# Optimization experiments

Measured on AMD Instinct MI355X. Metric: run time of the kernel, lower is better.

Reference implementation:

```python
import jax, jax.numpy as jnp
import numpy as np

HIDDEN = 1024   # hidden_dimensions (dim_in)
NUM_HEADS = 16
HEAD_DIM = 64   # dim_q == dim_k == output_dimensions per head
BATCH = 4
SEQ = 2048


def setup_inputs() -> dict:
    key = jax.random.key(0)
    ks = jax.random.split(key, 11)
    s = 1.0 / np.sqrt(HIDDEN)
    so = 1.0 / np.sqrt(NUM_HEADS * HEAD_DIM)
    return {
        "Q": jax.random.normal(ks[0], (BATCH, SEQ, HIDDEN), jnp.float32),
        "K": jax.random.normal(ks[1], (BATCH, SEQ, HIDDEN), jnp.float32),
        "V": jax.random.normal(ks[2], (BATCH, SEQ, HIDDEN), jnp.float32),
        # per-head projection weights stacked over the head axis
        "Wq": jax.random.uniform(ks[3], (NUM_HEADS, HIDDEN, HEAD_DIM), jnp.float32, -s, s),
        "bq": jax.random.uniform(ks[4], (NUM_HEADS, HEAD_DIM), jnp.float32, -s, s),
        "Wk": jax.random.uniform(ks[5], (NUM_HEADS, HIDDEN, HEAD_DIM), jnp.float32, -s, s),
        "bk": jax.random.uniform(ks[6], (NUM_HEADS, HEAD_DIM), jnp.float32, -s, s),
        "Wv": jax.random.uniform(ks[7], (NUM_HEADS, HIDDEN, HEAD_DIM), jnp.float32, -s, s),
        "bv": jax.random.uniform(ks[8], (NUM_HEADS, HEAD_DIM), jnp.float32, -s, s),
        # output projection: concat(num_heads*head_dim) -> hidden
        "Wo": jax.random.uniform(ks[9], (NUM_HEADS * HEAD_DIM, HIDDEN), jnp.float32, -so, so),
        "bo": jax.random.uniform(ks[10], (HIDDEN,), jnp.float32, -so, so),
    }


def reference(Q, K, V, Wq, bq, Wk, bk, Wv, bv, Wo, bo):
    # Per-head linear projections (batched over heads instead of Python loop)
    q = jnp.einsum("bsd,hdk->bhsk", Q, Wq) + bq[None, :, None, :]  # [B,H,S,dk]
    k = jnp.einsum("bsd,hdk->bhsk", K, Wk) + bk[None, :, None, :]
    v = jnp.einsum("bsd,hdk->bhsk", V, Wv) + bv[None, :, None, :]
    # Scaled dot-product attention
    scale = 1.0 / jnp.sqrt(jnp.asarray(k.shape[-1], q.dtype))
    scores = jnp.einsum("bhqk,bhsk->bhqs", q, k) * scale          # [B,H,S,S]
    attn = jax.nn.softmax(scores, axis=-1)
    o = jnp.einsum("bhqs,bhsk->bhqk", attn, v)                     # [B,H,S,dk]
    # Concatenate heads along the feature dim, then output linear
    B, H, S, dk = o.shape
    concat = jnp.transpose(o, (0, 2, 1, 3)).reshape(B, S, H * dk)  # [B,S,H*dk]
    return concat @ Wo + bo                                        # [B,S,HIDDEN]
```

## Files before the change

kernel.cpp:

```cpp
#include <hip/hip_runtime.h>
#include <hip/hip_bf16.h>
#include <stdint.h>

typedef unsigned short u16;
typedef uint32_t u32;
typedef __attribute__((ext_vector_type(4))) float f32x4;
typedef __attribute__((ext_vector_type(16))) float f32x16;
typedef __attribute__((ext_vector_type(8))) short s8v;
typedef __attribute__((ext_vector_type(4))) unsigned short u16x4;
typedef __attribute__((ext_vector_type(2))) uint32_t u32x2;

#define SCALE_Q 0.18033688f

__device__ __forceinline__ u16 f2bf(float f) {
  union { float f; uint32_t u; } v; v.f = f;
  uint32_t r = v.u + 0x7fffu + ((v.u >> 16) & 1u);
  return (u16)(r >> 16);
}

__device__ __forceinline__ u32 pk2(float lo, float hi) {
  __hip_bfloat162 h = __float22bfloat162_rn(float2{lo, hi});
  union { __hip_bfloat162 h; u32 u; } c; c.h = h; return c.u;
}

__device__ __forceinline__ void gl16(const void* g, void* l) {
  __builtin_amdgcn_global_load_lds((const __attribute__((address_space(1))) u32*)g,
                                   (__attribute__((address_space(3))) u32*)l, 16, 0, 0);
}

#define BARRIER()  __builtin_amdgcn_s_barrier()
#define SCHEDB()   __builtin_amdgcn_sched_barrier(0)

__global__ __launch_bounds__(256) void k_conv3(const float* __restrict__ a, const float* __restrict__ b,
                                               const float* __restrict__ c, u16* __restrict__ oa,
                                               u16* __restrict__ ob, u16* __restrict__ oc) {
  int which = blockIdx.y;
  const float* in = which == 0 ? a : (which == 1 ? b : c);
  u16* out = which == 0 ? oa : (which == 1 ? ob : oc);
  int i = (blockIdx.x * 256 + threadIdx.x) * 4;
  float4 v = *(const float4*)(in + i);
  u16x4 o; o[0] = f2bf(v.x); o[1] = f2bf(v.y); o[2] = f2bf(v.z); o[3] = f2bf(v.w);
  *(u16x4*)(out + i) = o;
}

__global__ __launch_bounds__(256) void k_convW_t(const float* __restrict__ wq, const float* __restrict__ wk,
                                                 const float* __restrict__ wv, u16* __restrict__ oq,
                                                 u16* __restrict__ ok, u16* __restrict__ ov) {
  __shared__ float T[64][65];
  const int z = blockIdx.z, h = blockIdx.y, d0 = blockIdx.x * 64;
  const float* w = z == 0 ? wq : (z == 1 ? wk : wv);
  u16* o = z == 0 ? oq : (z == 1 ? ok : ov);
  const float scale = z == 0 ? SCALE_Q : 1.0f;
  const int t = threadIdx.x;
#pragma unroll
  for (int i = 0; i < 16; ++i) {
    int f = t + i * 256;
    T[f >> 6][f & 63] = w[(h * 1024 + d0 + (f >> 6)) * 64 + (f & 63)];
  }
  __syncthreads();
#pragma unroll
  for (int i = 0; i < 16; ++i) {
    int g = t + i * 256;
    o[(h * 64 + (g >> 6)) * 1024 + d0 + (g & 63)] = f2bf(T[g & 63][g >> 6] * scale);
  }
}

__global__ __launch_bounds__(256) void k_convWo_t(const float* __restrict__ w, u16* __restrict__ o) {
  __shared__ float T[64][65];
  const int n0 = blockIdx.x * 64, c0 = blockIdx.y * 64;
  const int t = threadIdx.x;
#pragma unroll
  for (int i = 0; i < 16; ++i) {
    int f = t + i * 256;
    T[f >> 6][f & 63] = w[(c0 + (f >> 6)) * 1024 + n0 + (f & 63)];
  }
  __syncthreads();
#pragma unroll
  for (int i = 0; i < 16; ++i) {
    int g = t + i * 256;
    o[(n0 + (g >> 6)) * 1024 + c0 + (g & 63)] = f2bf(T[g & 63][g >> 6]);
  }
}

__global__ __launch_bounds__(256) void k_gemm3(
    const u16* __restrict__ Aq, const u16* __restrict__ Ak, const u16* __restrict__ Av,
    const u16* __restrict__ Bq, const u16* __restrict__ Bk, const u16* __restrict__ Bv,
    const float* __restrict__ bqp, const float* __restrict__ bkp, const float* __restrict__ bvp,
    u16* __restrict__ oq, u16* __restrict__ ok, u16* __restrict__ ov) {
  constexpr int Kd = 1024, Nd = 1024;
  __shared__ alignas(16) u16 As[2][128 * 64];
  __shared__ alignas(16) u16 Bs[2][128 * 64];
  const int z = blockIdx.z;
  const u16* A = z == 0 ? Aq : (z == 1 ? Ak : Av);
  const u16* Bt = z == 0 ? Bq : (z == 1 ? Bk : Bv);
  const float* bias = z == 0 ? bqp : (z == 1 ? bkp : bvp);

  const int t = threadIdx.x;
  const int lane = t & 63;
  const int w = t >> 6;
  const int wm = w >> 1, wn = w & 1;
  const int lr = lane & 15, lg = lane >> 4;
  const long bm = blockIdx.x * 128, bn = blockIdx.y * 128;
  const int r8 = lane >> 3, c8 = lane & 7;
  const int chunk = c8 ^ r8;

  f32x4 acc[4][4] = {};
  const u16* Ap = A + (bm + w * 8 + r8) * (long)Kd + chunk * 8;
  const u16* Bp = Bt + (bn + w * 8 + r8) * (long)Kd + chunk * 8;

  auto GSTAGE = [&](u16* Asb, u16* Bsb, int kt) {
#pragma unroll
    for (int p = 0; p < 4; ++p) {
      gl16(Ap + (long)p * 32 * Kd + kt, Asb + (p * 32 + w * 8) * 64);
      gl16(Bp + (long)p * 32 * Kd + kt, Bsb + (p * 32 + w * 8) * 64);
    }
  };
  auto GCOMP = [&](const u16* Asb, const u16* Bsb) {
#pragma unroll
    for (int ks = 0; ks < 2; ++ks) {
      s8v af[4], bf[4];
#pragma unroll
      for (int i = 0; i < 4; ++i) {
        int arow = wm * 64 + i * 16 + lr;
        af[i] = *(const s8v*)(Asb + arow * 64 + (((ks * 4 + lg) ^ (arow & 7)) * 8));
        int brow = wn * 64 + i * 16 + lr;
        bf[i] = *(const s8v*)(Bsb + brow * 64 + (((ks * 4 + lg) ^ (brow & 7)) * 8));
      }
#pragma unroll
      for (int i = 0; i < 4; ++i)
#pragma unroll
        for (int j = 0; j < 4; ++j)
          acc[i][j] = __builtin_amdgcn_mfma_f32_16x16x32_bf16(af[i], bf[j], acc[i][j], 0, 0, 0);
    }
  };

  GSTAGE(As[0], Bs[0], 0);
  for (int kt = 0; kt < 16; ++kt) {
    BARRIER();
    SCHEDB();
    if (kt < 15) {
      GSTAGE(As[(kt + 1) & 1], Bs[(kt + 1) & 1], (kt + 1) * 64);
      asm volatile("s_waitcnt vmcnt(8)" ::: "memory");
    } else {
      asm volatile("s_waitcnt vmcnt(0)" ::: "memory");
    }
    SCHEDB();
    BARRIER();
    SCHEDB();
    GCOMP(As[kt & 1], Bs[kt & 1]);
  }

  const float bscale = z == 0 ? SCALE_Q : 1.0f;
  float bcol[4];
#pragma unroll
  for (int j = 0; j < 4; ++j) bcol[j] = bias[bn + wn * 64 + j * 16 + lr] * bscale;

  if (z < 2) {
    u16* C = z == 0 ? oq : ok;
#pragma unroll
    for (int i = 0; i < 4; ++i) {
      long m0 = bm + wm * 64 + i * 16 + lg * 4;
#pragma unroll
      for (int j = 0; j < 4; ++j) {
        long n = bn + wn * 64 + j * 16 + lr;
#pragma unroll
        for (int r = 0; r < 4; ++r)
          C[(m0 + r) * Nd + n] = f2bf(acc[i][j][r] + bcol[j]);
      }
    }
  } else {
    u16* C = ov;
    int lgp = ((lg & 1) << 1) | (lg >> 1);
#pragma unroll
    for (int i = 0; i < 4; ++i) {
      long m0 = bm + wm * 64 + i * 16 + lgp * 4;
      int b = (int)(m0 >> 11), s0 = (int)(m0 & 2047);
#pragma unroll
      for (int j = 0; j < 4; ++j) {
        int n = (int)(bn + wn * 64 + j * 16 + lr);
        int h = n >> 6, dv = n & 63;
        u32x2 cc;
        cc[0] = pk2(acc[i][j][0] + bcol[j], acc[i][j][1] + bcol[j]);
        cc[1] = pk2(acc[i][j][2] + bcol[j], acc[i][j][3] + bcol[j]);
        *(u32x2*)(C + (long)((b * 16 + h) * 64 + dv) * 2048 + s0) = cc;
      }
    }
  }
}

__global__ __launch_bounds__(256) void k_gemmo(const u16* __restrict__ A, const u16* __restrict__ Bt,
                                               const float* __restrict__ bias, float* __restrict__ C) {
  constexpr int Kd = 1024, Nd = 1024;
  __shared__ alignas(16) u16 As[2][128 * 64];
  __shared__ alignas(16) u16 Bs[2][128 * 64];
  const int t = threadIdx.x;
  const int lane = t & 63;
  const int w = t >> 6;
  const int wm = w >> 1, wn = w & 1;
  const int lr = lane & 15, lg = lane >> 4;
  const long bm = blockIdx.x * 128, bn = blockIdx.y * 128;
  const int r8 = lane >> 3, c8 = lane & 7;
  const int chunk = c8 ^ r8;

  f32x4 acc[4][4] = {};
  const u16* Ap = A + (bm + w * 8 + r8) * (long)Kd + chunk * 8;
  const u16* Bp = Bt + (bn + w * 8 + r8) * (long)Kd + chunk * 8;

  auto GSTAGE = [&](u16* Asb, u16* Bsb, int kt) {
#pragma unroll
    for (int p = 0; p < 4; ++p) {
      gl16(Ap + (long)p * 32 * Kd + kt, Asb + (p * 32 + w * 8) * 64);
      gl16(Bp + (long)p * 32 * Kd + kt, Bsb + (p * 32 + w * 8) * 64);
    }
  };
  auto GCOMP = [&](const u16* Asb, const u16* Bsb) {
#pragma unroll
    for (int ks = 0; ks < 2; ++ks) {
      s8v af[4], bf[4];
#pragma unroll
      for (int i = 0; i < 4; ++i) {
        int arow = wm * 64 + i * 16 + lr;
        af[i] = *(const s8v*)(Asb + arow * 64 + (((ks * 4 + lg) ^ (arow & 7)) * 8));
        int brow = wn * 64 + i * 16 + lr;
        bf[i] = *(const s8v*)(Bsb + brow * 64 + (((ks * 4 + lg) ^ (brow & 7)) * 8));
      }
#pragma unroll
      for (int i = 0; i < 4; ++i)
#pragma unroll
        for (int j = 0; j < 4; ++j)
          acc[i][j] = __builtin_amdgcn_mfma_f32_16x16x32_bf16(af[i], bf[j], acc[i][j], 0, 0, 0);
    }
  };

  GSTAGE(As[0], Bs[0], 0);
  for (int kt = 0; kt < 16; ++kt) {
    BARRIER();
    SCHEDB();
    if (kt < 15) {
      GSTAGE(As[(kt + 1) & 1], Bs[(kt + 1) & 1], (kt + 1) * 64);
      asm volatile("s_waitcnt vmcnt(8)" ::: "memory");
    } else {
      asm volatile("s_waitcnt vmcnt(0)" ::: "memory");
    }
    SCHEDB();
    BARRIER();
    SCHEDB();
    GCOMP(As[kt & 1], Bs[kt & 1]);
  }

  float bcol[4];
#pragma unroll
  for (int j = 0; j < 4; ++j) bcol[j] = bias[bn + wn * 64 + j * 16 + lr];
#pragma unroll
  for (int i = 0; i < 4; ++i) {
    long m0 = bm + wm * 64 + i * 16 + lg * 4;
#pragma unroll
    for (int j = 0; j < 4; ++j) {
      long n = bn + wn * 64 + j * 16 + lr;
#pragma unroll
      for (int r = 0; r < 4; ++r)
        C[(m0 + r) * Nd + n] = acc[i][j][r] + bcol[j];
    }
  }
}

__global__ __launch_bounds__(256, 2) void k_attn(const u16* __restrict__ q, const u16* __restrict__ k,
                                                 const u16* __restrict__ vT, u16* __restrict__ o) {
  __shared__ alignas(16) u16 Ks[4][64 * 64];
  __shared__ alignas(16) u16 Vs[4][64 * 64];
  const int t = threadIdx.x;
  const int lane = t & 63;
  const int wv = t >> 6;
  const int l5 = lane & 31, hi = lane >> 5;
  const int r8 = lane >> 3, c8 = lane & 7;
  const int rx = l5 & 7;

  const int wg = blockIdx.x;
  const int ob = (wg & 7) * 64 + (wg >> 3);
  const int qt = ob & 7, h = (ob >> 3) & 15, b = ob >> 7;

  const int qrow0 = qt * 256 + wv * 64 + l5;
  const u16* qpA = q + ((long)(b * 2048 + qrow0) * 1024 + h * 64);
  const u16* qpB = qpA + 32 * 1024;
  s8v qfA[4], qfB[4];
#pragma unroll
  for (int s = 0; s < 4; ++s) {
    qfA[s] = *(const s8v*)(qpA + s * 16 + hi * 8);
    qfB[s] = *(const s8v*)(qpB + s * 16 + hi * 8);
  }

  const u16* Kpp = k + (long)b * 2048 * 1024 + h * 64 + (long)r8 * 1024 + ((c8 ^ r8) * 8);
  const u16* Vpp = vT + (long)(b * 16 + h) * 131072 + (long)r8 * 2048 + ((c8 ^ r8) * 8);

  f32x16 accA0 = {}, accA1 = {}, accB0 = {}, accB1 = {};
  float lA = 0.f, lB = 0.f;

  int offs[4];
#pragma unroll
  for (int s = 0; s < 4; ++s) offs[s] = ((2 * s + hi) ^ rx) * 8;
  const int rb0 = l5 * 64, rb1 = rb0 + 2048;

  auto ASTAGE = [&](int buf, int kv) {
#pragma unroll
    for (int r0 = 0; r0 < 2; ++r0) {
      int rowo = wv * 16 + r0 * 8;
      gl16(Kpp + ((long)kv + rowo) * 1024, &Ks[buf][rowo * 64]);
      gl16(Vpp + (long)rowo * 2048 + kv,   &Vs[buf][rowo * 64]);
    }
  };

  auto ATILE = [&](int buf) {
    const u16* Ksb = Ks[buf];
    const u16* Vsb = Vs[buf];
    s8v kf0[4], kf1[4];
#pragma unroll
    for (int s = 0; s < 4; ++s) {
      kf0[s] = *(const s8v*)(Ksb + rb0 + offs[s]);
      kf1[s] = *(const s8v*)(Ksb + rb1 + offs[s]);
    }
    f32x16 sA0 = {}, sA1 = {}, sB0 = {}, sB1 = {};
    __builtin_amdgcn_s_setprio(1);
#pragma unroll
    for (int s = 0; s < 4; ++s) {
      sA0 = __builtin_amdgcn_mfma_f32_32x32x16_bf16(kf0[s], qfA[s], sA0, 0, 0, 0);
      sA1 = __builtin_amdgcn_mfma_f32_32x32x16_bf16(kf1[s], qfA[s], sA1, 0, 0, 0);
      sB0 = __builtin_amdgcn_mfma_f32_32x32x16_bf16(kf0[s], qfB[s], sB0, 0, 0, 0);
      sB1 = __builtin_amdgcn_mfma_f32_32x32x16_bf16(kf1[s], qfB[s], sB1, 0, 0, 0);
    }
    __builtin_amdgcn_s_setprio(0);
    u32 PA[16], PB[16];
#pragma unroll
    for (int kb = 0; kb < 2; ++kb) {
#pragma unroll
      for (int r1 = 0; r1 < 4; ++r1) {
        float a0 = __builtin_amdgcn_exp2f(kb ? sA1[4 * r1 + 0] : sA0[4 * r1 + 0]);
        float a1 = __builtin_amdgcn_exp2f(kb ? sA1[4 * r1 + 1] : sA0[4 * r1 + 1]);
        float a2 = __builtin_amdgcn_exp2f(kb ? sA1[4 * r1 + 2] : sA0[4 * r1 + 2]);
        float a3 = __builtin_amdgcn_exp2f(kb ? sA1[4 * r1 + 3] : sA0[4 * r1 + 3]);
        lA += (a0 + a1) + (a2 + a3);
        PA[kb * 8 + r1 * 2 + 0] = pk2(a0, a1);
        PA[kb * 8 + r1 * 2 + 1] = pk2(a2, a3);
        float b0 = __builtin_amdgcn_exp2f(kb ? sB1[4 * r1 + 0] : sB0[4 * r1 + 0]);
        float b1 = __builtin_amdgcn_exp2f(kb ? sB1[4 * r1 + 1] : sB0[4 * r1 + 1]);
        float b2 = __builtin_amdgcn_exp2f(kb ? sB1[4 * r1 + 2] : sB0[4 * r1 + 2]);
        float b3 = __builtin_amdgcn_exp2f(kb ? sB1[4 * r1 + 3] : sB0[4 * r1 + 3]);
        lB += (b0 + b1) + (b2 + b3);
        PB[kb * 8 + r1 * 2 + 0] = pk2(b0, b1);
        PB[kb * 8 + r1 * 2 + 1] = pk2(b2, b3);
      }
    }
    __builtin_amdgcn_s_setprio(1);
#pragma unroll
    for (int s2 = 0; s2 < 4; ++s2) {
      union { s8v v; u32 w[4]; } pa, pb;
      pa.w[0] = PA[4 * s2 + 0]; pa.w[1] = PA[4 * s2 + 1];
      pa.w[2] = PA[4 * s2 + 2]; pa.w[3] = PA[4 * s2 + 3];
      pb.w[0] = PB[4 * s2 + 0]; pb.w[1] = PB[4 * s2 + 1];
      pb.w[2] = PB[4 * s2 + 2]; pb.w[3] = PB[4 * s2 + 3];
      s8v vf0 = *(const s8v*)(Vsb + rb0 + offs[s2]);
      s8v vf1 = *(const s8v*)(Vsb + rb1 + offs[s2]);
      accA0 = __builtin_amdgcn_mfma_f32_32x32x16_bf16(vf0, pa.v, accA0, 0, 0, 0);
      accA1 = __builtin_amdgcn_mfma_f32_32x32x16_bf16(vf1, pa.v, accA1, 0, 0, 0);
      accB0 = __builtin_amdgcn_mfma_f32_32x32x16_bf16(vf0, pb.v, accB0, 0, 0, 0);
      accB1 = __builtin_amdgcn_mfma_f32_32x32x16_bf16(vf1, pb.v, accB1, 0, 0, 0);
    }
    __builtin_amdgcn_s_setprio(0);
  };

  ASTAGE(0, 0);
  ASTAGE(1, 64);
  asm volatile("s_waitcnt vmcnt(4)" ::: "memory");
  SCHEDB();
  BARRIER();
  SCHEDB();
  for (int tt = 0; tt < 30; ++tt) {
    ASTAGE((tt + 2) & 3, (tt + 2) * 64);
    ATILE(tt & 3);
    asm volatile("s_waitcnt vmcnt(4) lgkmcnt(0)" ::: "memory");
    SCHEDB();
    BARRIER();
    SCHEDB();
  }
  ATILE(30 & 3);
  asm volatile("s_waitcnt vmcnt(0) lgkmcnt(0)" ::: "memory");
  SCHEDB();
  BARRIER();
  SCHEDB();
  ATILE(31 & 3);

  lA += __shfl_xor(lA, 32);
  lB += __shfl_xor(lB, 32);
  float iA = 1.0f / lA, iB = 1.0f / lB;
  u16* opA = o + ((long)(b * 2048 + qrow0) * 1024 + h * 64);
  u16* opB = opA + 32 * 1024;
#pragma unroll
  for (int kb = 0; kb < 2; ++kb) {
#pragma unroll
    for (int r1 = 0; r1 < 4; ++r1) {
      u32x2 ca, cb;
      float a0 = kb ? accA1[4 * r1 + 0] : accA0[4 * r1 + 0];
      float a1 = kb ? accA1[4 * r1 + 1] : accA0[4 * r1 + 1];
      float a2 = kb ? accA1[4 * r1 + 2] : accA0[4 * r1 + 2];
      float a3 = kb ? accA1[4 * r1 + 3] : accA0[4 * r1 + 3];
      ca[0] = pk2(a0 * iA, a1 * iA);
      ca[1] = pk2(a2 * iA, a3 * iA);
      *(u32x2*)(opA + kb * 32 + r1 * 8 + hi * 4) = ca;
      float b0 = kb ? accB1[4 * r1 + 0] : accB0[4 * r1 + 0];
      float b1 = kb ? accB1[4 * r1 + 1] : accB0[4 * r1 + 1];
      float b2 = kb ? accB1[4 * r1 + 2] : accB0[4 * r1 + 2];
      float b3 = kb ? accB1[4 * r1 + 3] : accB0[4 * r1 + 3];
      cb[0] = pk2(b0 * iB, b1 * iB);
      cb[1] = pk2(b2 * iB, b3 * iB);
      *(u32x2*)(opB + kb * 32 + r1 * 8 + hi * 4) = cb;
    }
  }
}

extern "C" void kernel_launch(void* const* d_in, const int* in_sizes, int n_in,
                              void* d_out, int out_size, void* d_ws, size_t ws_size,
                              hipStream_t stream) {
  const float* Q  = (const float*)d_in[0];
  const float* K  = (const float*)d_in[1];
  const float* V  = (const float*)d_in[2];
  const float* Wq = (const float*)d_in[3];
  const float* bq = (const float*)d_in[4];
  const float* Wk = (const float*)d_in[5];
  const float* bk = (const float*)d_in[6];
  const float* Wv = (const float*)d_in[7];
  const float* bvp = (const float*)d_in[8];
  const float* Wo = (const float*)d_in[9];
  const float* bo = (const float*)d_in[10];
  float* out = (float*)d_out;

  char* ws = (char*)d_ws;
  const size_t MB16 = (size_t)8192 * 1024 * 2;
  u16* Qb  = (u16*)(ws);
  u16* Kb  = (u16*)(ws + MB16);
  u16* Vb  = (u16*)(ws + 2 * MB16);
  u16* WqT = (u16*)(ws + 3 * MB16);
  u16* WkT = (u16*)(ws + 3 * MB16 + ((size_t)2 << 20));
  u16* WvT = (u16*)(ws + 3 * MB16 + ((size_t)4 << 20));
  u16* WoT = (u16*)(ws + 3 * MB16 + ((size_t)6 << 20));
  u16* qws = (u16*)(ws + 3 * MB16 + ((size_t)8 << 20));
  u16* kws = (u16*)(ws + 4 * MB16 + ((size_t)8 << 20));
  u16* vTs = (u16*)(ws + 5 * MB16 + ((size_t)8 << 20));
  u16* ows = Qb;

  k_conv3<<<dim3(8192, 3), 256, 0, stream>>>(Q, K, V, Qb, Kb, Vb);
  k_convW_t<<<dim3(16, 16, 3), 256, 0, stream>>>(Wq, Wk, Wv, WqT, WkT, WvT);
  k_convWo_t<<<dim3(16, 16), 256, 0, stream>>>(Wo, WoT);

  k_gemm3<<<dim3(64, 8, 3), 256, 0, stream>>>(Qb, Kb, Vb, WqT, WkT, WvT,
                                              bq, bk, bvp, qws, kws, vTs);

  k_attn<<<dim3(512), 256, 0, stream>>>(qws, kws, vTs, ows);

  k_gemmo<<<dim3(64, 8), 256, 0, stream>>>(ows, WoT, bo, out);
}
```

Baseline: 204.7 us.

## Interleave softmax exp with MFMA groups inside attention tile via sched_group_barrier

Splits each attention tile into halves so the exp2/pack work of one half of the score block overlaps the MFMAs of the other half (the second QK^T half and the first PV half). sched_group_barrier masks pin the mix of MFMA, VALU and LDS-read instructions. V fragments are loaded up front and the setprio calls are dropped. The aim is to hide the exp VALU latency behind matrix-core work, at the cost of higher register pressure and a fragile dependence on compiler scheduling.

```diff
diff --git a/kernel.cpp b/kernel.cpp
--- a/kernel.cpp
+++ b/kernel.cpp
@@ -12,6 +12,8 @@
 
 #define SCALE_Q 0.18033688f
 
+union PU { s8v v; u32 w[4]; };
+
 __device__ __forceinline__ u16 f2bf(float f) {
   union { float f; uint32_t u; } v; v.f = f;
   uint32_t r = v.u + 0x7fffu + ((v.u >> 16) & 1u);
@@ -30,6 +32,7 @@
 
 #define BARRIER()  __builtin_amdgcn_s_barrier()
 #define SCHEDB()   __builtin_amdgcn_sched_barrier(0)
+#define SGB(m, n)  __builtin_amdgcn_sched_group_barrier((m), (n), 0)
 
 __global__ __launch_bounds__(256) void k_conv3(const float* __restrict__ a, const float* __restrict__ b,
                                                const float* __restrict__ c, u16* __restrict__ oa,
@@ -309,62 +312,78 @@
     }
   };
 
+  auto EXPPACK = [&](const f32x16& sv, PU& u0, PU& u1, float& l) {
+#pragma unroll
+    for (int r1 = 0; r1 < 4; ++r1) {
+      float p0 = __builtin_amdgcn_exp2f(sv[4 * r1 + 0]);
+      float p1 = __builtin_amdgcn_exp2f(sv[4 * r1 + 1]);
+      float p2 = __builtin_amdgcn_exp2f(sv[4 * r1 + 2]);
+      float p3 = __builtin_amdgcn_exp2f(sv[4 * r1 + 3]);
+      l += (p0 + p1) + (p2 + p3);
+      if (r1 < 2) {
+        u0.w[(r1 & 1) * 2 + 0] = pk2(p0, p1);
+        u0.w[(r1 & 1) * 2 + 1] = pk2(p2, p3);
+      } else {
+        u1.w[(r1 & 1) * 2 + 0] = pk2(p0, p1);
+        u1.w[(r1 & 1) * 2 + 1] = pk2(p2, p3);
+      }
+    }
+  };
+
   auto ATILE = [&](int buf) {
     const u16* Ksb = Ks[buf];
     const u16* Vsb = Vs[buf];
+    PU paU[4], pbU[4];
+    f32x16 sA0 = {}, sB0 = {}, sA1 = {}, sB1 = {};
     s8v kf0[4], kf1[4];
 #pragma unroll
     for (int s = 0; s < 4; ++s) {
       kf0[s] = *(const s8v*)(Ksb + rb0 + offs[s]);
       kf1[s] = *(const s8v*)(Ksb + rb1 + offs[s]);
     }
-    f32x16 sA0 = {}, sA1 = {}, sB0 = {}, sB1 = {};
-    __builtin_amdgcn_s_setprio(1);
 #pragma unroll
     for (int s = 0; s < 4; ++s) {
       sA0 = __builtin_amdgcn_mfma_f32_32x32x16_bf16(kf0[s], qfA[s], sA0, 0, 0, 0);
+      sB0 = __builtin_amdgcn_mfma_f32_32x32x16_bf16(kf0[s], qfB[s], sB0, 0, 0, 0);
+    }
+#pragma unroll
+    for (int g = 0; g < 4; ++g) { SGB(0x100, 2); SGB(0x8, 2); }
+    SCHEDB();
+#pragma unroll
+    for (int s = 0; s < 4; ++s) {
       sA1 = __builtin_amdgcn_mfma_f32_32x32x16_bf16(kf1[s], qfA[s], sA1, 0, 0, 0);
-      sB0 = __builtin_amdgcn_mfma_f32_32x32x16_bf16(kf0[s], qfB[s], sB0, 0, 0, 0);
       sB1 = __builtin_amdgcn_mfma_f32_32x32x16_bf16(kf1[s], qfB[s], sB1, 0, 0, 0);
     }
-    __builtin_amdgcn_s_setprio(0);
-    u32 PA[16], PB[16];
-#pragma unroll
-    for (int kb = 0; kb < 2; ++kb) {
-#pragma unroll
-      for (int r1 = 0; r1 < 4; ++r1) {
-        float a0 = __builtin_amdgcn_exp2f(kb ? sA1[4 * r1 + 0] : sA0[4 * r1 + 0]);
-        float a1 = __builtin_amdgcn_exp2f(kb ? sA1[4 * r1 + 1] : sA0[4 * r1 + 1]);
-        float a2 = __builtin_amdgcn_exp2f(kb ? sA1[4 * r1 + 2] : sA0[4 * r1 + 2]);
-        float a3 = __builtin_amdgcn_exp2f(kb ? sA1[4 * r1 + 3] : sA0[4 * r1 + 3]);
-        lA += (a0 + a1) + (a2 + a3);
-        PA[kb * 8 + r1 * 2 + 0] = pk2(a0, a1);
-        PA[kb * 8 + r1 * 2 + 1] = pk2(a2, a3);
-        float b0 = __builtin_amdgcn_exp2f(kb ? sB1[4 * r1 + 0] : sB0[4 * r1 + 0]);
-        float b1 = __builtin_amdgcn_exp2f(kb ? sB1[4 * r1 + 1] : sB0[4 * r1 + 1]);
-        float b2 = __builtin_amdgcn_exp2f(kb ? sB1[4 * r1 + 2] : sB0[4 * r1 + 2]);
-        float b3 = __builtin_amdgcn_exp2f(kb ? sB1[4 * r1 + 3] : sB0[4 * r1 + 3]);
-        lB += (b0 + b1) + (b2 + b3);
-        PB[kb * 8 + r1 * 2 + 0] = pk2(b0, b1);
-        PB[kb * 8 + r1 * 2 + 1] = pk2(b2, b3);
-      }
-    }
-    __builtin_amdgcn_s_setprio(1);
-#pragma unroll
-    for (int s2 = 0; s2 < 4; ++s2) {
-      union { s8v v; u32 w[4]; } pa, pb;
-      pa.w[0] = PA[4 * s2 + 0]; pa.w[1] = PA[4 * s2 + 1];
-      pa.w[2] = PA[4 * s2 + 2]; pa.w[3] = PA[4 * s2 + 3];
-      pb.w[0] = PB[4 * s2 + 0]; pb.w[1] = PB[4 * s2 + 1];
-      pb.w[2] = PB[4 * s2 + 2]; pb.w[3] = PB[4 * s2 + 3];
-      s8v vf0 = *(const s8v*)(Vsb + rb0 + offs[s2]);
-      s8v vf1 = *(const s8v*)(Vsb + rb1 + offs[s2]);
-      accA0 = __builtin_amdgcn_mfma_f32_32x32x16_bf16(vf0, pa.v, accA0, 0, 0, 0);
-      accA1 = __builtin_amdgcn_mfma_f32_32x32x16_bf16(vf1, pa.v, accA1, 0, 0, 0);
-      accB0 = __builtin_amdgcn_mfma_f32_32x32x16_bf16(vf0, pb.v, accB0, 0, 0, 0);
-      accB1 = __builtin_amdgcn_mfma_f32_32x32x16_bf16(vf1, pb.v, accB1, 0, 0, 0);
-    }
-    __builtin_amdgcn_s_setprio(0);
+    EXPPACK(sA0, paU[0], paU[1], lA);
+    EXPPACK(sB0, pbU[0], pbU[1], lB);
+#pragma unroll
+    for (int g = 0; g < 8; ++g) { SGB(0x8, 1); SGB(0x2, 9); }
+    SCHEDB();
+    s8v vf0[4], vf1[4];
+#pragma unroll
+    for (int s = 0; s < 4; ++s) {
+      vf0[s] = *(const s8v*)(Vsb + rb0 + offs[s]);
+      vf1[s] = *(const s8v*)(Vsb + rb1 + offs[s]);
+    }
+#pragma unroll
+    for (int s2 = 0; s2 < 2; ++s2) {
+      accA0 = __builtin_amdgcn_mfma_f32_32x32x16_bf16(vf0[s2], paU[s2].v, accA0, 0, 0, 0);
+      accA1 = __builtin_amdgcn_mfma_f32_32x32x16_bf16(vf1[s2], paU[s2].v, accA1, 0, 0, 0);
+      accB0 = __builtin_amdgcn_mfma_f32_32x32x16_bf16(vf0[s2], pbU[s2].v, accB0, 0, 0, 0);
+      accB1 = __builtin_amdgcn_mfma_f32_32x32x16_bf16(vf1[s2], pbU[s2].v, accB1, 0, 0, 0);
+    }
+    EXPPACK(sA1, paU[2], paU[3], lA);
+    EXPPACK(sB1, pbU[2], pbU[3], lB);
+#pragma unroll
+    for (int g = 0; g < 8; ++g) { SGB(0x100, 1); SGB(0x8, 1); SGB(0x2, 9); }
+    SCHEDB();
+#pragma unroll
+    for (int s2 = 2; s2 < 4; ++s2) {
+      accA0 = __builtin_amdgcn_mfma_f32_32x32x16_bf16(vf0[s2], paU[s2].v, accA0, 0, 0, 0);
+      accA1 = __builtin_amdgcn_mfma_f32_32x32x16_bf16(vf1[s2], paU[s2].v, accA1, 0, 0, 0);
+      accB0 = __builtin_amdgcn_mfma_f32_32x32x16_bf16(vf0[s2], pbU[s2].v, accB0, 0, 0, 0);
+      accB1 = __builtin_amdgcn_mfma_f32_32x32x16_bf16(vf1[s2], pbU[s2].v, accB1, 0, 0, 0);
+    }
   };
 
   ASTAGE(0, 0);
```

New measurement: 200.8 us. About the same (-1.9%).

## Load K/V fragments directly from global into registers, dropping LDS staging

Applied to the files above, without the earlier changes.

The attention kernel stops staging K and V tiles in LDS through async global-to-LDS copies and barriers. Each wave now loads its own K and V MFMA fragments straight from global memory into registers, double-buffered over 32-key chunks. This removes LDS traffic and block-wide barriers. The cost is that all four waves of a block redundantly fetch the same K/V data from global/L2, with less coalesced 16-byte row-strided accesses and more register pressure.

```diff
diff --git a/kernel.cpp b/kernel.cpp
--- a/kernel.cpp
+++ b/kernel.cpp
@@ -11,6 +11,8 @@
 typedef __attribute__((ext_vector_type(2))) uint32_t u32x2;
 
 #define SCALE_Q 0.18033688f
+
+union PU { s8v v; u32 w[4]; };
 
 __device__ __forceinline__ u16 f2bf(float f) {
   union { float f; uint32_t u; } v; v.f = f;
@@ -266,14 +268,10 @@
 
 __global__ __launch_bounds__(256, 2) void k_attn(const u16* __restrict__ q, const u16* __restrict__ k,
                                                  const u16* __restrict__ vT, u16* __restrict__ o) {
-  __shared__ alignas(16) u16 Ks[4][64 * 64];
-  __shared__ alignas(16) u16 Vs[4][64 * 64];
   const int t = threadIdx.x;
   const int lane = t & 63;
   const int wv = t >> 6;
   const int l5 = lane & 31, hi = lane >> 5;
-  const int r8 = lane >> 3, c8 = lane & 7;
-  const int rx = l5 & 7;
 
   const int wg = blockIdx.x;
   const int ob = (wg & 7) * 64 + (wg >> 3);
@@ -289,104 +287,67 @@
     qfB[s] = *(const s8v*)(qpB + s * 16 + hi * 8);
   }
 
-  const u16* Kpp = k + (long)b * 2048 * 1024 + h * 64 + (long)r8 * 1024 + ((c8 ^ r8) * 8);
-  const u16* Vpp = vT + (long)(b * 16 + h) * 131072 + (long)r8 * 2048 + ((c8 ^ r8) * 8);
+  const u16* Kl = k + (long)b * 2048 * 1024 + h * 64 + (long)l5 * 1024 + hi * 8;
+  const u16* Vl = vT + (long)(b * 16 + h) * 131072 + (long)l5 * 2048 + hi * 8;
 
   f32x16 accA0 = {}, accA1 = {}, accB0 = {}, accB1 = {};
   float lA = 0.f, lB = 0.f;
 
-  int offs[4];
-#pragma unroll
-  for (int s = 0; s < 4; ++s) offs[s] = ((2 * s + hi) ^ rx) * 8;
-  const int rb0 = l5 * 64, rb1 = rb0 + 2048;
-
-  auto ASTAGE = [&](int buf, int kv) {
-#pragma unroll
-    for (int r0 = 0; r0 < 2; ++r0) {
-      int rowo = wv * 16 + r0 * 8;
-      gl16(Kpp + ((long)kv + rowo) * 1024, &Ks[buf][rowo * 64]);
-      gl16(Vpp + (long)rowo * 2048 + kv,   &Vs[buf][rowo * 64]);
-    }
-  };
-
-  auto ATILE = [&](int buf) {
-    const u16* Ksb = Ks[buf];
-    const u16* Vsb = Vs[buf];
-    s8v kf0[4], kf1[4];
+  struct KV { s8v kf[4]; s8v vf[2][2]; };
+  KV b0, b1;
+
+  auto LOAD = [&](KV& bb, int kv0) {
+#pragma unroll
+    for (int s = 0; s < 4; ++s)
+      bb.kf[s] = *(const s8v*)(Kl + (long)kv0 * 1024 + s * 16);
+#pragma unroll
+    for (int d = 0; d < 2; ++d)
+#pragma unroll
+      for (int s2 = 0; s2 < 2; ++s2)
+        bb.vf[d][s2] = *(const s8v*)(Vl + d * 65536 + kv0 + s2 * 16);
+  };
+
+  auto COMPUTE = [&](const KV& bb) {
+    f32x16 sA = {}, sB = {};
 #pragma unroll
     for (int s = 0; s < 4; ++s) {
-      kf0[s] = *(const s8v*)(Ksb + rb0 + offs[s]);
-      kf1[s] = *(const s8v*)(Ksb + rb1 + offs[s]);
-    }
-    f32x16 sA0 = {}, sA1 = {}, sB0 = {}, sB1 = {};
-    __builtin_amdgcn_s_setprio(1);
-#pragma unroll
-    for (int s = 0; s < 4; ++s) {
-      sA0 = __builtin_amdgcn_mfma_f32_32x32x16_bf16(kf0[s], qfA[s], sA0, 0, 0, 0);
-      sA1 = __builtin_amdgcn_mfma_f32_32x32x16_bf16(kf1[s], qfA[s], sA1, 0, 0, 0);
-      sB0 = __builtin_amdgcn_mfma_f32_32x32x16_bf16(kf0[s], qfB[s], sB0, 0, 0, 0);
-      sB1 = __builtin_amdgcn_mfma_f32_32x32x16_bf16(kf1[s], qfB[s], sB1, 0, 0, 0);
-    }
-    __builtin_amdgcn_s_setprio(0);
-    u32 PA[16], PB[16];
-#pragma unroll
-    for (int kb = 0; kb < 2; ++kb) {
-#pragma unroll
-      for (int r1 = 0; r1 < 4; ++r1) {
-        float a0 = __builtin_amdgcn_exp2f(kb ? sA1[4 * r1 + 0] : sA0[4 * r1 + 0]);
-        float a1 = __builtin_amdgcn_exp2f(kb ? sA1[4 * r1 + 1] : sA0[4 * r1 + 1]);
-        float a2 = __builtin_amdgcn_exp2f(kb ? sA1[4 * r1 + 2] : sA0[4 * r1 + 2]);
-        float a3 = __builtin_amdgcn_exp2f(kb ? sA1[4 * r1 + 3] : sA0[4 * r1 + 3]);
-        lA += (a0 + a1) + (a2 + a3);
-        PA[kb * 8 + r1 * 2 + 0] = pk2(a0, a1);
-        PA[kb * 8 + r1 * 2 + 1] = pk2(a2, a3);
-        float b0 = __builtin_amdgcn_exp2f(kb ? sB1[4 * r1 + 0] : sB0[4 * r1 + 0]);
-        float b1 = __builtin_amdgcn_exp2f(kb ? sB1[4 * r1 + 1] : sB0[4 * r1 + 1]);
-        float b2 = __builtin_amdgcn_exp2f(kb ? sB1[4 * r1 + 2] : sB0[4 * r1 + 2]);
-        float b3 = __builtin_amdgcn_exp2f(kb ? sB1[4 * r1 + 3] : sB0[4 * r1 + 3]);
-        lB += (b0 + b1) + (b2 + b3);
-        PB[kb * 8 + r1 * 2 + 0] = pk2(b0, b1);
-        PB[kb * 8 + r1 * 2 + 1] = pk2(b2, b3);
-      }
-    }
-    __builtin_amdgcn_s_setprio(1);
-#pragma unroll
-    for (int s2 = 0; s2 < 4; ++s2) {
-      union { s8v v; u32 w[4]; } pa, pb;
-      pa.w[0] = PA[4 * s2 + 0]; pa.w[1] = PA[4 * s2 + 1];
-      pa.w[2] = PA[4 * s2 + 2]; pa.w[3] = PA[4 * s2 + 3];
-      pb.w[0] = PB[4 * s2 + 0]; pb.w[1] = PB[4 * s2 + 1];
-      pb.w[2] = PB[4 * s2 + 2]; pb.w[3] = PB[4 * s2 + 3];
-      s8v vf0 = *(const s8v*)(Vsb + rb0 + offs[s2]);
-      s8v vf1 = *(const s8v*)(Vsb + rb1 + offs[s2]);
-      accA0 = __builtin_amdgcn_mfma_f32_32x32x16_bf16(vf0, pa.v, accA0, 0, 0, 0);
-      accA1 = __builtin_amdgcn_mfma_f32_32x32x16_bf16(vf1, pa.v, accA1, 0, 0, 0);
-      accB0 = __builtin_amdgcn_mfma_f32_32x32x16_bf16(vf0, pb.v, accB0, 0, 0, 0);
-      accB1 = __builtin_amdgcn_mfma_f32_32x32x16_bf16(vf1, pb.v, accB1, 0, 0, 0);
-    }
-    __builtin_amdgcn_s_setprio(0);
-  };
-
-  ASTAGE(0, 0);
-  ASTAGE(1, 64);
-  asm volatile("s_waitcnt vmcnt(4)" ::: "memory");
-  SCHEDB();
-  BARRIER();
-  SCHEDB();
-  for (int tt = 0; tt < 30; ++tt) {
-    ASTAGE((tt + 2) & 3, (tt + 2) * 64);
-    ATILE(tt & 3);
-    asm volatile("s_waitcnt vmcnt(4) lgkmcnt(0)" ::: "memory");
-    SCHEDB();
-    BARRIER();
-    SCHEDB();
-  }
-  ATILE(30 & 3);
-  asm volatile("s_waitcnt vmcnt(0) lgkmcnt(0)" ::: "memory");
-  SCHEDB();
-  BARRIER();
-  SCHEDB();
-  ATILE(31 & 3);
+      sA = __builtin_amdgcn_mfma_f32_32x32x16_bf16(bb.kf[s], qfA[s], sA, 0, 0, 0);
+      sB = __builtin_amdgcn_mfma_f32_32x32x16_bf16(bb.kf[s], qfB[s], sB, 0, 0, 0);
+    }
+    PU pA[2], pB[2];
+#pragma unroll
+    for (int r1 = 0; r1 < 4; ++r1) {
+      float a0 = __builtin_amdgcn_exp2f(sA[4 * r1 + 0]);
+      float a1 = __builtin_amdgcn_exp2f(sA[4 * r1 + 1]);
+      float a2 = __builtin_amdgcn_exp2f(sA[4 * r1 + 2]);
+      float a3 = __builtin_amdgcn_exp2f(sA[4 * r1 + 3]);
+      lA += (a0 + a1) + (a2 + a3);
+      pA[r1 >> 1].w[(r1 & 1) * 2 + 0] = pk2(a0, a1);
+      pA[r1 >> 1].w[(r1 & 1) * 2 + 1] = pk2(a2, a3);
+      float c0 = __builtin_amdgcn_exp2f(sB[4 * r1 + 0]);
+      float c1 = __builtin_amdgcn_exp2f(sB[4 * r1 + 1]);
+      float c2 = __builtin_amdgcn_exp2f(sB[4 * r1 + 2]);
+      float c3 = __builtin_amdgcn_exp2f(sB[4 * r1 + 3]);
+      lB += (c0 + c1) + (c2 + c3);
+      pB[r1 >> 1].w[(r1 & 1) * 2 + 0] = pk2(c0, c1);
+      pB[r1 >> 1].w[(r1 & 1) * 2 + 1] = pk2(c2, c3);
+    }
+#pragma unroll
+    for (int s2 = 0; s2 < 2; ++s2) {
+      accA0 = __builtin_amdgcn_mfma_f32_32x32x16_bf16(bb.vf[0][s2], pA[s2].v, accA0, 0, 0, 0);
+      accA1 = __builtin_amdgcn_mfma_f32_32x32x16_bf16(bb.vf[1][s2], pA[s2].v, accA1, 0, 0, 0);
+      accB0 = __builtin_amdgcn_mfma_f32_32x32x16_bf16(bb.vf[0][s2], pB[s2].v, accB0, 0, 0, 0);
+      accB1 = __builtin_amdgcn_mfma_f32_32x32x16_bf16(bb.vf[1][s2], pB[s2].v, accB1, 0, 0, 0);
+    }
+  };
+
+  LOAD(b0, 0);
+  for (int it = 0; it < 64; it += 2) {
+    LOAD(b1, (it + 1) * 32);
+    COMPUTE(b0);
+    if (it + 2 < 64) LOAD(b0, (it + 2) * 32);
+    COMPUTE(b1);
+  }
 
   lA += __shfl_xor(lA, 32);
   lB += __shfl_xor(lB, 32);
@@ -405,12 +366,12 @@
       ca[0] = pk2(a0 * iA, a1 * iA);
       ca[1] = pk2(a2 * iA, a3 * iA);
       *(u32x2*)(opA + kb * 32 + r1 * 8 + hi * 4) = ca;
-      float b0 = kb ? accB1[4 * r1 + 0] : accB0[4 * r1 + 0];
-      float b1 = kb ? accB1[4 * r1 + 1] : accB0[4 * r1 + 1];
-      float b2 = kb ? accB1[4 * r1 + 2] : accB0[4 * r1 + 2];
-      float b3 = kb ? accB1[4 * r1 + 3] : accB0[4 * r1 + 3];
-      cb[0] = pk2(b0 * iB, b1 * iB);
-      cb[1] = pk2(b2 * iB, b3 * iB);
+      float b0v = kb ? accB1[4 * r1 + 0] : accB0[4 * r1 + 0];
+      float b1v = kb ? accB1[4 * r1 + 1] : accB0[4 * r1 + 1];
+      float b2v = kb ? accB1[4 * r1 + 2] : accB0[4 * r1 + 2];
+      float b3v = kb ? accB1[4 * r1 + 3] : accB0[4 * r1 + 3];
+      cb[0] = pk2(b0v * iB, b1v * iB);
+      cb[1] = pk2(b2v * iB, b3v * iB);
       *(u32x2*)(opB + kb * 32 + r1 * 8 + hi * 4) = cb;
     }
   }
```

After: 245.6 us. +20.0%, slower.
